# Optimization experiments

Hardware: AMD Instinct MI355X
Metric: run time of the kernel (lower is better)

The kernel has to match this reference:

```python
import jax, jax.numpy as jnp
import numpy as np

N_NODES = 50000
N_EDGES = 800000
IN_FEATS, HIDDEN, NUM_CLASSES = 64, 128, 64


def setup_inputs() -> dict:
    key = jax.random.key(0)
    ks = jax.random.split(key, 7)
    features = jax.random.normal(ks[0], (N_NODES, IN_FEATS), dtype=jnp.float32)
    # Glorot-ish scaled weights, zero bias (DGL GraphConv default bias init is zeros)
    W1 = jax.random.normal(ks[1], (IN_FEATS, HIDDEN), dtype=jnp.float32) / np.sqrt(IN_FEATS)
    b1 = jnp.zeros((HIDDEN,), dtype=jnp.float32)
    W2 = jax.random.normal(ks[2], (HIDDEN, NUM_CLASSES), dtype=jnp.float32) / np.sqrt(HIDDEN)
    b2 = jnp.zeros((NUM_CLASSES,), dtype=jnp.float32)
    src = jax.random.randint(ks[3], (N_EDGES,), 0, N_NODES, dtype=jnp.int32)
    dst = jax.random.randint(ks[4], (N_EDGES,), 0, N_NODES, dtype=jnp.int32)
    return {"features": features, "W1": W1, "b1": b1, "W2": W2, "b2": b2,
            "src": src, "dst": dst}


def reference(features, W1, b1, W2, b2, src, dst):
    N = features.shape[0]
    ones = jnp.ones(src.shape[0], dtype=features.dtype)
    in_deg = jax.ops.segment_sum(ones, dst, num_segments=N)   # [N]
    out_deg = jax.ops.segment_sum(ones, src, num_segments=N)  # [N]
    norm_in = jnp.maximum(in_deg, 1.0) ** -0.5    # clamp(min=1)^{-1/2}
    norm_out = jnp.maximum(out_deg, 1.0) ** -0.5

    def graph_conv(feat, W, b):
        # DGL GraphConv, norm='both': src-scale, SpMM sum, dst-scale, linear.
        h = feat * norm_out[:, None]
        if feat.shape[1] > W.shape[1]:
            # mult W first (in_feats > out_feats) -> aggregate in smaller dim
            h = h @ W
            agg = jax.ops.segment_sum(h[src], dst, num_segments=N)
            return agg * norm_in[:, None] + b
        else:
            agg = jax.ops.segment_sum(h[src], dst, num_segments=N)
            return (agg * norm_in[:, None]) @ W + b

    manual_norm = norm_in[:, None]                 # module's extra in-deg^{-1/2}
    x = features * manual_norm
    h = jax.nn.relu(graph_conv(x, W1, b1))
    h = h * manual_norm
    out = graph_conv(h, W2, b2)                    # single etype -> mean is identity
    return out
```

## Files before the change

kernel.cpp:

```cpp
#include <hip/hip_runtime.h>

#define NNODES 50000
#define NEDGES 800000
#define IN_F 64
#define HID 128
#define OUT_F 64
#define STRIDE 64
#define NPB 256
#define NB 196
#define BCAP 5120
#define CHUNK 2048

typedef __attribute__((ext_vector_type(8))) short bf16x8;
typedef __attribute__((ext_vector_type(4))) float f32x4;

static __device__ __forceinline__ unsigned short f2bf(float f) {
    unsigned int u = __float_as_uint(f);
    u = u + 0x7FFFu + ((u >> 16) & 1u);
    return (unsigned short)(u >> 16);
}
static __device__ __forceinline__ float bf2f(unsigned short h) {
    return __uint_as_float((unsigned int)h << 16);
}
static __device__ __forceinline__ unsigned int packbf(float a, float b) {
    return (unsigned int)f2bf(a) | ((unsigned int)f2bf(b) << 16);
}

__global__ __launch_bounds__(256) void prep_wt(const float* __restrict__ W1,
                                               const float* __restrict__ W2,
                                               unsigned short* __restrict__ W1t,
                                               unsigned short* __restrict__ W2t,
                                               int* __restrict__ bcur) {
    const int i0 = blockIdx.x * 256 + threadIdx.x;
    const int str = gridDim.x * 256;
    if (blockIdx.x == 0)
        for (int i = threadIdx.x; i < 2 * NB; i += 256) bcur[i] = 0;
    for (int i = i0; i < 64 * 128; i += str) {
        int k = i >> 7, c = i & 127;
        W1t[c * 72 + k] = f2bf(W1[i]);
    }
    for (int i = i0; i < 128 * 64; i += str) {
        int k = i >> 6, c = i & 63;
        W2t[c * 136 + k] = f2bf(W2[i]);
    }
}


__global__ __launch_bounds__(256) void bucket_edges_k(const int* __restrict__ src,
                                                      const int* __restrict__ dst,
                                                      int* __restrict__ bcur_d,
                                                      int* __restrict__ bcur_s,
                                                      unsigned int* __restrict__ bed,
                                                      unsigned char* __restrict__ bes) {
    __shared__ int cntd[NB], cnts[NB], based_[NB], bases_[NB];
    const int tid = threadIdx.x;
    const int e0 = blockIdx.x * CHUNK;
    for (int i = tid; i < NB; i += 256) { cntd[i] = 0; cnts[i] = 0; }
    __syncthreads();
    for (int k = tid; k < CHUNK; k += 256) {
        int e = e0 + k;
        if (e < NEDGES) {
            atomicAdd(&cntd[dst[e] >> 8], 1);
            atomicAdd(&cnts[src[e] >> 8], 1);
        }
    }
    __syncthreads();
    for (int i = tid; i < NB; i += 256) {
        based_[i] = cntd[i] ? atomicAdd(&bcur_d[i], cntd[i]) : 0;
        bases_[i] = cnts[i] ? atomicAdd(&bcur_s[i], cnts[i]) : 0;
        cntd[i] = 0; cnts[i] = 0;
    }
    __syncthreads();
    for (int k = tid; k < CHUNK; k += 256) {
        int e = e0 + k;
        if (e < NEDGES) {
            int s = src[e], d = dst[e];
            int bd = d >> 8, bs = s >> 8;
            int pd = based_[bd] + atomicAdd(&cntd[bd], 1);
            if (pd < BCAP) bed[(size_t)bd * BCAP + pd] = ((unsigned)s << 8) | (unsigned)(d & 255);
            int ps = bases_[bs] + atomicAdd(&cnts[bs], 1);
            if (ps < BCAP) bes[(size_t)bs * BCAP + ps] = (unsigned char)(s & 255);
        }
    }
}

__global__ __launch_bounds__(256) void csr_norm_xpre(const int* __restrict__ bcur_d,
                                                     const int* __restrict__ bcur_s,
                                                     const unsigned int* __restrict__ bed,
                                                     const unsigned char* __restrict__ bes,
                                                     const float* __restrict__ feat,
                                                     unsigned short* __restrict__ padded,
                                                     int* __restrict__ deg_in,
                                                     float* __restrict__ norm_in,
                                                     float* __restrict__ sc,
                                                     unsigned short* __restrict__ xbf) {
    __shared__ int curs[NPB];
    __shared__ int hist[NPB];
    __shared__ float scl[NPB];
    const int b = blockIdx.x;
    const int tid = threadIdx.x;
    const int base = b << 8;
    curs[tid] = 0; hist[tid] = 0;
    __syncthreads();
    const int nd = min(bcur_d[b], BCAP);
    const int ns = min(bcur_s[b], BCAP);
    const unsigned int* ed = bed + (size_t)b * BCAP;
    const unsigned char* es = bes + (size_t)b * BCAP;
    for (int k = tid; k < nd; k += 256) {
        unsigned v = ed[k];
        int s = (int)(v >> 8), dl = (int)(v & 255u);
        int pos = atomicAdd(&curs[dl], 1);
        if (pos < STRIDE) padded[((size_t)(base + dl) << 6) + pos] = (unsigned short)s;
    }
    for (int k = tid; k < ns; k += 256)
        atomicAdd(&hist[(int)es[k]], 1);
    __syncthreads();
    int node = base + tid;
    if (node < NNODES) {
        int din = curs[tid];
        int dout = hist[tid];
        deg_in[node] = din;
        if (din < 1) din = 1;
        if (dout < 1) dout = 1;
        float ni = 1.0f / sqrtf((float)din);
        float no = 1.0f / sqrtf((float)dout);
        norm_in[node] = ni;
        float s_ = ni * no;
        sc[node] = s_;
        scl[tid] = s_;
    } else {
        scl[tid] = 0.0f;
    }
    __syncthreads();
    const float4* f4 = (const float4*)feat;
    for (int i = tid; i < NPB * 16; i += 256) {
        int nl = i >> 4;
        int gn = base + nl;
        if (gn < NNODES) {
            float4 v = f4[(size_t)gn * 16 + (i & 15)];
            float s_ = scl[nl];
            ushort4 o;
            o.x = f2bf(v.x * s_); o.y = f2bf(v.y * s_);
            o.z = f2bf(v.z * s_); o.w = f2bf(v.w * s_);
            *(ushort4*)&xbf[((size_t)gn << 6) + (size_t)(i & 15) * 4] = o;
        }
    }
}


__global__ __launch_bounds__(256) void agg_xpre(const int* __restrict__ deg_in,
                                                const unsigned short* __restrict__ padded,
                                                const unsigned short* __restrict__ xbf,
                                                unsigned short* __restrict__ aggb) {
    const int tid = threadIdx.x;
    const int node = blockIdx.x * 16 + (tid >> 4);
    const int sl = tid & 15;
    if (node >= NNODES) return;
    const unsigned short* row = padded + ((size_t)node << 6);
    int n = deg_in[node]; if (n > STRIDE) n = STRIDE;
    float4 A0 = {0,0,0,0}, A1 = {0,0,0,0}, A2 = {0,0,0,0}, A3 = {0,0,0,0};
    int k = 0;
    for (; k + 4 <= n; k += 4) {
        const uint2 rr = *(const uint2*)&row[k];
        const int s0 = rr.x & 0xffff, s1 = rr.x >> 16;
        const int s2 = rr.y & 0xffff, s3 = rr.y >> 16;
        ushort4 a = *(const ushort4*)&xbf[((size_t)s0 << 6) + (size_t)sl * 4];
        ushort4 b = *(const ushort4*)&xbf[((size_t)s1 << 6) + (size_t)sl * 4];
        ushort4 c = *(const ushort4*)&xbf[((size_t)s2 << 6) + (size_t)sl * 4];
        ushort4 d = *(const ushort4*)&xbf[((size_t)s3 << 6) + (size_t)sl * 4];
        A0.x += bf2f(a.x); A0.y += bf2f(a.y); A0.z += bf2f(a.z); A0.w += bf2f(a.w);
        A1.x += bf2f(b.x); A1.y += bf2f(b.y); A1.z += bf2f(b.z); A1.w += bf2f(b.w);
        A2.x += bf2f(c.x); A2.y += bf2f(c.y); A2.z += bf2f(c.z); A2.w += bf2f(c.w);
        A3.x += bf2f(d.x); A3.y += bf2f(d.y); A3.z += bf2f(d.z); A3.w += bf2f(d.w);
    }
    for (; k < n; ++k) {
        const int s = row[k];
        ushort4 a = *(const ushort4*)&xbf[((size_t)s << 6) + (size_t)sl * 4];
        A0.x += bf2f(a.x); A0.y += bf2f(a.y); A0.z += bf2f(a.z); A0.w += bf2f(a.w);
    }
    ushort4 o;
    o.x = f2bf((A0.x + A1.x) + (A2.x + A3.x));
    o.y = f2bf((A0.y + A1.y) + (A2.y + A3.y));
    o.z = f2bf((A0.z + A1.z) + (A2.z + A3.z));
    o.w = f2bf((A0.w + A1.w) + (A2.w + A3.w));
    *(ushort4*)&aggb[((size_t)node << 6) + (size_t)sl * 4] = o;
}

__global__ __launch_bounds__(256) void agg_final(const int* __restrict__ deg_in,
                                                 const unsigned short* __restrict__ padded,
                                                 const unsigned short* __restrict__ Pb,
                                                 const float* __restrict__ norm_in,
                                                 const float* __restrict__ b2,
                                                 float* __restrict__ out) {
    const int tid = threadIdx.x;
    const int node = blockIdx.x * 16 + (tid >> 4);
    const int sl = tid & 15;
    if (node >= NNODES) return;
    const unsigned short* row = padded + ((size_t)node << 6);
    int n = deg_in[node]; if (n > STRIDE) n = STRIDE;
    float4 A0 = {0,0,0,0}, A1 = {0,0,0,0}, A2 = {0,0,0,0}, A3 = {0,0,0,0};
    int k = 0;
    for (; k + 4 <= n; k += 4) {
        const uint2 rr = *(const uint2*)&row[k];
        const int s0 = rr.x & 0xffff, s1 = rr.x >> 16;
        const int s2 = rr.y & 0xffff, s3 = rr.y >> 16;
        ushort4 a = *(const ushort4*)&Pb[((size_t)s0 << 6) + (size_t)sl * 4];
        ushort4 b = *(const ushort4*)&Pb[((size_t)s1 << 6) + (size_t)sl * 4];
        ushort4 c = *(const ushort4*)&Pb[((size_t)s2 << 6) + (size_t)sl * 4];
        ushort4 d = *(const ushort4*)&Pb[((size_t)s3 << 6) + (size_t)sl * 4];
        A0.x += bf2f(a.x); A0.y += bf2f(a.y); A0.z += bf2f(a.z); A0.w += bf2f(a.w);
        A1.x += bf2f(b.x); A1.y += bf2f(b.y); A1.z += bf2f(b.z); A1.w += bf2f(b.w);
        A2.x += bf2f(c.x); A2.y += bf2f(c.y); A2.z += bf2f(c.z); A2.w += bf2f(c.w);
        A3.x += bf2f(d.x); A3.y += bf2f(d.y); A3.z += bf2f(d.z); A3.w += bf2f(d.w);
    }
    for (; k < n; ++k) {
        const int s = row[k];
        ushort4 a = *(const ushort4*)&Pb[((size_t)s << 6) + (size_t)sl * 4];
        A0.x += bf2f(a.x); A0.y += bf2f(a.y); A0.z += bf2f(a.z); A0.w += bf2f(a.w);
    }
    const float ni = norm_in[node];
    const float4 bb = *(const float4*)&b2[sl * 4];
    float4 r;
    r.x = fmaf((A0.x + A1.x) + (A2.x + A3.x), ni, bb.x);
    r.y = fmaf((A0.y + A1.y) + (A2.y + A3.y), ni, bb.y);
    r.z = fmaf((A0.z + A1.z) + (A2.z + A3.z), ni, bb.z);
    r.w = fmaf((A0.w + A1.w) + (A2.w + A3.w), ni, bb.w);
    *(float4*)&out[((size_t)node << 6) + (size_t)sl * 4] = r;
}

__global__ __launch_bounds__(256) void gemm12_mfma(const unsigned short* __restrict__ AGGb,
                                                   const unsigned short* __restrict__ W1t,
                                                   const float* __restrict__ b1,
                                                   const unsigned short* __restrict__ W2t,
                                                   const float* __restrict__ norm_in,
                                                   const float* __restrict__ sc,
                                                   unsigned short* __restrict__ Pout) {
    __shared__ unsigned short lds[17408];
    unsigned int* lds32 = (unsigned int*)lds;
    const int tid = threadIdx.x;
    const int block0 = blockIdx.x * 64;
    const int lane = tid & 63;
    const int w = tid >> 6;
    const int r16 = lane & 15;
    const int kq = lane >> 4;

    const unsigned int* aggu = (const unsigned int*)AGGb;
    for (int i = tid; i < 64 * 32; i += 256) {
        int row = i >> 5, kp = i & 31;
        int gn = block0 + row; if (gn >= NNODES) gn = NNODES - 1;
        lds32[row * 36 + kp] = aggu[(size_t)gn * 32 + kp];
    }
    for (int i = tid; i < 4608; i += 256)
        lds32[2304 + i] = ((const unsigned int*)W1t)[i];
    __syncthreads();

    f32x4 acc[8];
#pragma unroll
    for (int n = 0; n < 8; ++n) acc[n] = (f32x4){0.f, 0.f, 0.f, 0.f};
    const bf16x8 a0 = *(const bf16x8*)&lds[(w * 16 + r16) * 72 + kq * 8];
    const bf16x8 a1 = *(const bf16x8*)&lds[(w * 16 + r16) * 72 + 32 + kq * 8];
#pragma unroll
    for (int n = 0; n < 8; ++n) {
        const bf16x8 b0 = *(const bf16x8*)&lds[4608 + (n * 16 + r16) * 72 + kq * 8];
        const bf16x8 b1f = *(const bf16x8*)&lds[4608 + (n * 16 + r16) * 72 + 32 + kq * 8];
        acc[n] = __builtin_amdgcn_mfma_f32_16x16x32_bf16(a0, b0, acc[n], 0, 0, 0);
        acc[n] = __builtin_amdgcn_mfma_f32_16x16x32_bf16(a1, b1f, acc[n], 0, 0, 0);
    }
    __syncthreads();

    {
        const int hbase = w * 2176;
#pragma unroll
        for (int i = 0; i < 4; ++i) {
            int node = block0 + w * 16 + kq * 4 + i;
            int cn = node < NNODES ? node : NNODES - 1;
            const float ni = norm_in[cn], s = sc[cn];
#pragma unroll
            for (int n = 0; n < 8; ++n) {
                const int col = n * 16 + r16;
                const float h = fmaxf(fmaf(acc[n][i], ni, b1[col]), 0.0f) * s;
                lds[hbase + (kq * 4 + i) * 136 + col] = f2bf(h);
            }
        }
    }
    for (int i = tid; i < 4352; i += 256)
        lds32[4352 + i] = ((const unsigned int*)W2t)[i];
    __syncthreads();

    f32x4 acc2[4];
#pragma unroll
    for (int n = 0; n < 4; ++n) acc2[n] = (f32x4){0.f, 0.f, 0.f, 0.f};
#pragma unroll
    for (int kc = 0; kc < 4; ++kc) {
        const bf16x8 a = *(const bf16x8*)&lds[w * 2176 + r16 * 136 + kc * 32 + kq * 8];
#pragma unroll
        for (int n = 0; n < 4; ++n) {
            const bf16x8 b = *(const bf16x8*)&lds[8704 + (n * 16 + r16) * 136 + kc * 32 + kq * 8];
            acc2[n] = __builtin_amdgcn_mfma_f32_16x16x32_bf16(a, b, acc2[n], 0, 0, 0);
        }
    }

#pragma unroll
    for (int i = 0; i < 4; ++i) {
        const int node = block0 + w * 16 + kq * 4 + i;
        if (node < NNODES) {
#pragma unroll
            for (int n = 0; n < 4; ++n)
                Pout[((size_t)node << 6) + n * 16 + r16] = f2bf(acc2[n][i]);
        }
    }
}


static inline size_t align_up(size_t x, size_t a) { return (x + a - 1) & ~(a - 1); }

extern "C" void kernel_launch(void* const* d_in, const int* in_sizes, int n_in,
                              void* d_out, int out_size, void* d_ws, size_t ws_size,
                              hipStream_t stream) {
    const float* features = (const float*)d_in[0];
    const float* W1       = (const float*)d_in[1];
    const float* b1       = (const float*)d_in[2];
    const float* W2       = (const float*)d_in[3];
    const float* b2       = (const float*)d_in[4];
    const int*   src      = (const int*)d_in[5];
    const int*   dst      = (const int*)d_in[6];
    float* out = (float*)d_out;

    char* ws = (char*)d_ws;
    size_t off = 0;
    int*   bcur     = (int*)(ws + off);   off = align_up(off + 2 * NB * sizeof(int), 256);
    int*   bcur_d   = bcur;
    int*   bcur_s   = bcur + NB;
    int*   deg_in   = (int*)(ws + off);   off = align_up(off + NNODES * sizeof(int), 256);
    float* norm_in  = (float*)(ws + off); off = align_up(off + NNODES * sizeof(float), 256);
    float* sc       = (float*)(ws + off); off = align_up(off + NNODES * sizeof(float), 256);
    unsigned short* padded = (unsigned short*)(ws + off);
    off = align_up(off + (size_t)NNODES * STRIDE * sizeof(unsigned short), 256);
    unsigned short* AGGb = (unsigned short*)(ws + off);
    off = align_up(off + (size_t)NNODES * IN_F * sizeof(unsigned short), 256);
    float* C        = (float*)(ws + off); off = align_up(off + (size_t)NNODES * HID * sizeof(float), 256);
    unsigned int*   bed = (unsigned int*)C;
    unsigned char*  bes = (unsigned char*)((char*)C + align_up((size_t)NB * BCAP * 4, 256));
    unsigned short* xbf = (unsigned short*)((char*)C + (8u << 20));
    unsigned short* Pb  = (unsigned short*)C;
    unsigned short* W1t = (unsigned short*)((char*)C + (16u << 20));
    unsigned short* W2t = W1t + 128 * 72;
    (void)ws_size; (void)out_size; (void)n_in; (void)in_sizes;

    const int B256 = 256;

    prep_wt<<<16, B256, 0, stream>>>(W1, W2, W1t, W2t, bcur);
    bucket_edges_k<<<(NEDGES + CHUNK - 1) / CHUNK, B256, 0, stream>>>(src, dst, bcur_d, bcur_s, bed, bes);
    csr_norm_xpre<<<NB, B256, 0, stream>>>(bcur_d, bcur_s, bed, bes, features,
                                           padded, deg_in, norm_in, sc, xbf);
    agg_xpre<<<(NNODES + 15) / 16, B256, 0, stream>>>(deg_in, padded, xbf, AGGb);
    gemm12_mfma<<<(NNODES + 63) / 64, B256, 0, stream>>>(AGGb, W1t, b1, W2t, norm_in, sc, Pb);
    agg_final<<<(NNODES + 15) / 16, B256, 0, stream>>>(deg_in, padded, Pb, norm_in, b2, out);
}
```

Before: 100.7 us.

## Split gathered feature tables into two column-half planes for L2 locality

The bf16 node feature tables gathered by both aggregation kernels are stored as two separate 32-column planes. Each aggregation then runs as two launches, one per plane, with 8 threads per node. The intent is to shrink the randomly gathered working set per launch so it fits in L2 and the gathers hit cache more often. In exchange, the neighbor index lists and degrees are read twice, two extra kernel launches are added, and each gathered row segment is narrower.

```diff
diff --git a/kernel.cpp b/kernel.cpp
--- a/kernel.cpp
+++ b/kernel.cpp
@@ -93,7 +93,8 @@
                                                      int* __restrict__ deg_in,
                                                      float* __restrict__ norm_in,
                                                      float* __restrict__ sc,
-                                                     unsigned short* __restrict__ xbf) {
+                                                     unsigned short* __restrict__ xbf0,
+                                                     unsigned short* __restrict__ xbf1) {
     __shared__ int curs[NPB];
     __shared__ int hist[NPB];
     __shared__ float scl[NPB];
@@ -135,14 +136,18 @@
     const float4* f4 = (const float4*)feat;
     for (int i = tid; i < NPB * 16; i += 256) {
         int nl = i >> 4;
+        int q = i & 15;
         int gn = base + nl;
         if (gn < NNODES) {
-            float4 v = f4[(size_t)gn * 16 + (i & 15)];
+            float4 v = f4[(size_t)gn * 16 + q];
             float s_ = scl[nl];
             ushort4 o;
             o.x = f2bf(v.x * s_); o.y = f2bf(v.y * s_);
             o.z = f2bf(v.z * s_); o.w = f2bf(v.w * s_);
-            *(ushort4*)&xbf[((size_t)gn << 6) + (size_t)(i & 15) * 4] = o;
+            if (q < 8)
+                *(ushort4*)&xbf0[((size_t)gn << 5) + (size_t)q * 4] = o;
+            else
+                *(ushort4*)&xbf1[((size_t)gn << 5) + (size_t)(q - 8) * 4] = o;
         }
     }
 }
@@ -150,11 +155,12 @@
 
 __global__ __launch_bounds__(256) void agg_xpre(const int* __restrict__ deg_in,
                                                 const unsigned short* __restrict__ padded,
-                                                const unsigned short* __restrict__ xbf,
-                                                unsigned short* __restrict__ aggb) {
-    const int tid = threadIdx.x;
-    const int node = blockIdx.x * 16 + (tid >> 4);
-    const int sl = tid & 15;
+                                                const unsigned short* __restrict__ plane,
+                                                unsigned short* __restrict__ aggb,
+                                                int H) {
+    const int tid = threadIdx.x;
+    const int node = blockIdx.x * 32 + (tid >> 3);
+    const int sl = tid & 7;
     if (node >= NNODES) return;
     const unsigned short* row = padded + ((size_t)node << 6);
     int n = deg_in[node]; if (n > STRIDE) n = STRIDE;
@@ -164,10 +170,10 @@
         const uint2 rr = *(const uint2*)&row[k];
         const int s0 = rr.x & 0xffff, s1 = rr.x >> 16;
         const int s2 = rr.y & 0xffff, s3 = rr.y >> 16;
-        ushort4 a = *(const ushort4*)&xbf[((size_t)s0 << 6) + (size_t)sl * 4];
-        ushort4 b = *(const ushort4*)&xbf[((size_t)s1 << 6) + (size_t)sl * 4];
-        ushort4 c = *(const ushort4*)&xbf[((size_t)s2 << 6) + (size_t)sl * 4];
-        ushort4 d = *(const ushort4*)&xbf[((size_t)s3 << 6) + (size_t)sl * 4];
+        ushort4 a = *(const ushort4*)&plane[((size_t)s0 << 5) + (size_t)sl * 4];
+        ushort4 b = *(const ushort4*)&plane[((size_t)s1 << 5) + (size_t)sl * 4];
+        ushort4 c = *(const ushort4*)&plane[((size_t)s2 << 5) + (size_t)sl * 4];
+        ushort4 d = *(const ushort4*)&plane[((size_t)s3 << 5) + (size_t)sl * 4];
         A0.x += bf2f(a.x); A0.y += bf2f(a.y); A0.z += bf2f(a.z); A0.w += bf2f(a.w);
         A1.x += bf2f(b.x); A1.y += bf2f(b.y); A1.z += bf2f(b.z); A1.w += bf2f(b.w);
         A2.x += bf2f(c.x); A2.y += bf2f(c.y); A2.z += bf2f(c.z); A2.w += bf2f(c.w);
@@ -175,7 +181,7 @@
     }
     for (; k < n; ++k) {
         const int s = row[k];
-        ushort4 a = *(const ushort4*)&xbf[((size_t)s << 6) + (size_t)sl * 4];
+        ushort4 a = *(const ushort4*)&plane[((size_t)s << 5) + (size_t)sl * 4];
         A0.x += bf2f(a.x); A0.y += bf2f(a.y); A0.z += bf2f(a.z); A0.w += bf2f(a.w);
     }
     ushort4 o;
@@ -183,18 +189,19 @@
     o.y = f2bf((A0.y + A1.y) + (A2.y + A3.y));
     o.z = f2bf((A0.z + A1.z) + (A2.z + A3.z));
     o.w = f2bf((A0.w + A1.w) + (A2.w + A3.w));
-    *(ushort4*)&aggb[((size_t)node << 6) + (size_t)sl * 4] = o;
+    *(ushort4*)&aggb[((size_t)node << 6) + (size_t)(H * 32 + sl * 4)] = o;
 }
 
 __global__ __launch_bounds__(256) void agg_final(const int* __restrict__ deg_in,
                                                  const unsigned short* __restrict__ padded,
-                                                 const unsigned short* __restrict__ Pb,
+                                                 const unsigned short* __restrict__ plane,
                                                  const float* __restrict__ norm_in,
                                                  const float* __restrict__ b2,
-                                                 float* __restrict__ out) {
-    const int tid = threadIdx.x;
-    const int node = blockIdx.x * 16 + (tid >> 4);
-    const int sl = tid & 15;
+                                                 float* __restrict__ out,
+                                                 int H) {
+    const int tid = threadIdx.x;
+    const int node = blockIdx.x * 32 + (tid >> 3);
+    const int sl = tid & 7;
     if (node >= NNODES) return;
     const unsigned short* row = padded + ((size_t)node << 6);
     int n = deg_in[node]; if (n > STRIDE) n = STRIDE;
@@ -204,10 +211,10 @@
         const uint2 rr = *(const uint2*)&row[k];
         const int s0 = rr.x & 0xffff, s1 = rr.x >> 16;
         const int s2 = rr.y & 0xffff, s3 = rr.y >> 16;
-        ushort4 a = *(const ushort4*)&Pb[((size_t)s0 << 6) + (size_t)sl * 4];
-        ushort4 b = *(const ushort4*)&Pb[((size_t)s1 << 6) + (size_t)sl * 4];
-        ushort4 c = *(const ushort4*)&Pb[((size_t)s2 << 6) + (size_t)sl * 4];
-        ushort4 d = *(const ushort4*)&Pb[((size_t)s3 << 6) + (size_t)sl * 4];
+        ushort4 a = *(const ushort4*)&plane[((size_t)s0 << 5) + (size_t)sl * 4];
+        ushort4 b = *(const ushort4*)&plane[((size_t)s1 << 5) + (size_t)sl * 4];
+        ushort4 c = *(const ushort4*)&plane[((size_t)s2 << 5) + (size_t)sl * 4];
+        ushort4 d = *(const ushort4*)&plane[((size_t)s3 << 5) + (size_t)sl * 4];
         A0.x += bf2f(a.x); A0.y += bf2f(a.y); A0.z += bf2f(a.z); A0.w += bf2f(a.w);
         A1.x += bf2f(b.x); A1.y += bf2f(b.y); A1.z += bf2f(b.z); A1.w += bf2f(b.w);
         A2.x += bf2f(c.x); A2.y += bf2f(c.y); A2.z += bf2f(c.z); A2.w += bf2f(c.w);
@@ -215,17 +222,18 @@
     }
     for (; k < n; ++k) {
         const int s = row[k];
-        ushort4 a = *(const ushort4*)&Pb[((size_t)s << 6) + (size_t)sl * 4];
+        ushort4 a = *(const ushort4*)&plane[((size_t)s << 5) + (size_t)sl * 4];
         A0.x += bf2f(a.x); A0.y += bf2f(a.y); A0.z += bf2f(a.z); A0.w += bf2f(a.w);
     }
     const float ni = norm_in[node];
-    const float4 bb = *(const float4*)&b2[sl * 4];
+    const int col = H * 32 + sl * 4;
+    const float4 bb = *(const float4*)&b2[col];
     float4 r;
     r.x = fmaf((A0.x + A1.x) + (A2.x + A3.x), ni, bb.x);
     r.y = fmaf((A0.y + A1.y) + (A2.y + A3.y), ni, bb.y);
     r.z = fmaf((A0.z + A1.z) + (A2.z + A3.z), ni, bb.z);
     r.w = fmaf((A0.w + A1.w) + (A2.w + A3.w), ni, bb.w);
-    *(float4*)&out[((size_t)node << 6) + (size_t)sl * 4] = r;
+    *(float4*)&out[((size_t)node << 6) + col] = r;
 }
 
 __global__ __launch_bounds__(256) void gemm12_mfma(const unsigned short* __restrict__ AGGb,
@@ -234,7 +242,8 @@
                                                    const unsigned short* __restrict__ W2t,
                                                    const float* __restrict__ norm_in,
                                                    const float* __restrict__ sc,
-                                                   unsigned short* __restrict__ Pout) {
+                                                   unsigned short* __restrict__ Pb0,
+                                                   unsigned short* __restrict__ Pb1) {
     __shared__ unsigned short lds[17408];
     unsigned int* lds32 = (unsigned int*)lds;
     const int tid = threadIdx.x;
@@ -304,9 +313,10 @@
     for (int i = 0; i < 4; ++i) {
         const int node = block0 + w * 16 + kq * 4 + i;
         if (node < NNODES) {
-#pragma unroll
-            for (int n = 0; n < 4; ++n)
-                Pout[((size_t)node << 6) + n * 16 + r16] = f2bf(acc2[n][i]);
+            Pb0[((size_t)node << 5) + 0 * 16 + r16] = f2bf(acc2[0][i]);
+            Pb0[((size_t)node << 5) + 1 * 16 + r16] = f2bf(acc2[1][i]);
+            Pb1[((size_t)node << 5) + 0 * 16 + r16] = f2bf(acc2[2][i]);
+            Pb1[((size_t)node << 5) + 1 * 16 + r16] = f2bf(acc2[3][i]);
         }
     }
 }
@@ -339,21 +349,27 @@
     unsigned short* AGGb = (unsigned short*)(ws + off);
     off = align_up(off + (size_t)NNODES * IN_F * sizeof(unsigned short), 256);
     float* C        = (float*)(ws + off); off = align_up(off + (size_t)NNODES * HID * sizeof(float), 256);
-    unsigned int*   bed = (unsigned int*)C;
-    unsigned char*  bes = (unsigned char*)((char*)C + align_up((size_t)NB * BCAP * 4, 256));
-    unsigned short* xbf = (unsigned short*)((char*)C + (8u << 20));
-    unsigned short* Pb  = (unsigned short*)C;
-    unsigned short* W1t = (unsigned short*)((char*)C + (16u << 20));
-    unsigned short* W2t = W1t + 128 * 72;
+    const size_t PLANE = (size_t)NNODES * 32 * sizeof(unsigned short);
+    unsigned int*   bed  = (unsigned int*)C;
+    unsigned char*  bes  = (unsigned char*)((char*)C + align_up((size_t)NB * BCAP * 4, 256));
+    unsigned short* Pb0  = (unsigned short*)C;
+    unsigned short* Pb1  = (unsigned short*)((char*)C + PLANE);
+    unsigned short* xbf0 = (unsigned short*)((char*)C + (8u << 20));
+    unsigned short* xbf1 = (unsigned short*)((char*)C + (8u << 20) + PLANE);
+    unsigned short* W1t  = (unsigned short*)((char*)C + (16u << 20));
+    unsigned short* W2t  = W1t + 128 * 72;
     (void)ws_size; (void)out_size; (void)n_in; (void)in_sizes;
 
     const int B256 = 256;
+    const int AGG_GRID = (NNODES + 31) / 32;
 
     prep_wt<<<16, B256, 0, stream>>>(W1, W2, W1t, W2t, bcur);
     bucket_edges_k<<<(NEDGES + CHUNK - 1) / CHUNK, B256, 0, stream>>>(src, dst, bcur_d, bcur_s, bed, bes);
     csr_norm_xpre<<<NB, B256, 0, stream>>>(bcur_d, bcur_s, bed, bes, features,
-                                           padded, deg_in, norm_in, sc, xbf);
-    agg_xpre<<<(NNODES + 15) / 16, B256, 0, stream>>>(deg_in, padded, xbf, AGGb);
-    gemm12_mfma<<<(NNODES + 63) / 64, B256, 0, stream>>>(AGGb, W1t, b1, W2t, norm_in, sc, Pb);
-    agg_final<<<(NNODES + 15) / 16, B256, 0, stream>>>(deg_in, padded, Pb, norm_in, b2, out);
-}
+                                           padded, deg_in, norm_in, sc, xbf0, xbf1);
+    agg_xpre<<<AGG_GRID, B256, 0, stream>>>(deg_in, padded, xbf0, AGGb, 0);
+    agg_xpre<<<AGG_GRID, B256, 0, stream>>>(deg_in, padded, xbf1, AGGb, 1);
+    gemm12_mfma<<<(NNODES + 63) / 64, B256, 0, stream>>>(AGGb, W1t, b1, W2t, norm_in, sc, Pb0, Pb1);
+    agg_final<<<AGG_GRID, B256, 0, stream>>>(deg_in, padded, Pb0, norm_in, b2, out, 0);
+    agg_final<<<AGG_GRID, B256, 0, stream>>>(deg_in, padded, Pb1, norm_in, b2, out, 1);
+}
```

After: 113.3 us. 12.6% more time.
